# Kernel tuning notes

Measured on AMD Instinct MI355X. Metric: run time of the kernel, lower is better.

The kernel has to match this reference:

```python
import jax, jax.numpy as jnp
import numpy as np

GRID_SIZE = 5
K = 3  # spline order
WIDTH = [512, 1024, 1024, 1024, 256]
BATCH = 4096


def make_grid(in_dim):
    # pykan-style extended uniform grid on [-1, 1]: G + 2K + 1 knots per input dim
    h = 2.0 / GRID_SIZE
    pts = jnp.arange(-K, GRID_SIZE + K + 1, dtype=jnp.float32) * h - 1.0
    return jnp.tile(pts[None, :], (in_dim, 1))


def bspline_basis(x, grid):
    # Cox-de Boor recursion. x: [B, in], grid: [in, G+2K+1] -> basis [B, in, G+K]
    xe = x[..., None]
    b = ((xe >= grid[:, :-1]) & (xe < grid[:, 1:])).astype(x.dtype)  # degree 0: [B, in, G+2K]
    for d in range(1, K + 1):
        left = (xe - grid[:, :-(d + 1)]) / (grid[:, d:-1] - grid[:, :-(d + 1)]) * b[..., :-1]
        right = (grid[:, d + 1:] - xe) / (grid[:, d + 1:] - grid[:, 1:-d]) * b[..., 1:]
        b = left + right
    return b


def kan_layer(x, grid, coef, scale_base, scale_sp):
    # out_j = sum_i scale_base[i,j]*silu(x_i) + scale_sp[i,j]*sum_g coef[i,j,g]*B_g(x_i)
    basis = bspline_basis(x, grid)                                   # [B, in, G+K]
    base = jnp.einsum('bi,io->bo', jax.nn.silu(x), scale_base)
    spline = jnp.einsum('big,iog->bo', basis, coef * scale_sp[:, :, None])
    return base + spline


def setup_inputs() -> dict:
    key = jax.random.key(0)
    n_layers = len(WIDTH) - 1
    keys = jax.random.split(key, 2 + 2 * n_layers)
    inp = {
        'inputs_y': jax.random.normal(keys[0], (BATCH, 256), dtype=jnp.float32) * 0.5,
        'inputs_u': jax.random.normal(keys[1], (BATCH, 256), dtype=jnp.float32) * 0.5,
    }
    for l, (din, dout) in enumerate(zip(WIDTH[:-1], WIDTH[1:])):
        inp[f'coef{l}'] = jax.random.normal(keys[2 + 2 * l], (din, dout, GRID_SIZE + K), dtype=jnp.float32) * (0.1 / np.sqrt(din))
        inp[f'sb{l}'] = jax.random.normal(keys[3 + 2 * l], (din, dout), dtype=jnp.float32) * (1.0 / np.sqrt(din))
        inp[f'ss{l}'] = jnp.ones((din, dout), dtype=jnp.float32)
        inp[f'grid{l}'] = make_grid(din)
    return inp


def reference(inputs_y, inputs_u,
              coef0, sb0, ss0, grid0,
              coef1, sb1, ss1, grid1,
              coef2, sb2, ss2, grid2,
              coef3, sb3, ss3, grid3):
    x = jnp.concatenate([inputs_y.astype(jnp.float32), inputs_u.astype(jnp.float32)], axis=-1)
    layers = [(grid0, coef0, sb0, ss0), (grid1, coef1, sb1, ss1),
              (grid2, coef2, sb2, ss2), (grid3, coef3, sb3, ss3)]
    for g, c, sb, ss in layers:
        x = kan_layer(x, g, c, sb, ss)
    return x
```

## Files before the change

### kernel.cpp

```cpp
#include <hip/hip_runtime.h>
#include <cstdint>
#include <cstddef>

typedef _Float16 f16;
typedef _Float16 f16x4 __attribute__((ext_vector_type(4)));
typedef _Float16 f16x8 __attribute__((ext_vector_type(8)));
typedef float f32x4 __attribute__((ext_vector_type(4)));

__device__ __forceinline__ void gl2lds16(const void* g, void* l) {
  __builtin_amdgcn_global_load_lds(
      (const __attribute__((address_space(1))) void*)(uintptr_t)g,
      (__attribute__((address_space(3))) void*)(uintptr_t)l,
      16, 0, 0);
}

__global__ __launch_bounds__(256) void kan_prep2(
    const float* __restrict__ coef, const float* __restrict__ sb,
    const float* __restrict__ ss, f16* __restrict__ Wt,
    int out, int K9)
{
  __shared__ float s_sb[32][32];
  __shared__ float s_ss[32][32];
  __shared__ f16 s_w[32][288];
  const int t  = threadIdx.x;
  const int o0 = blockIdx.x * 32, i0 = blockIdx.y * 32;

  {
    int il = t >> 3, oc = (t & 7) * 4;
    float4 vb = *(const float4*)(sb + (size_t)(i0 + il) * out + o0 + oc);
    float4 vs = *(const float4*)(ss + (size_t)(i0 + il) * out + o0 + oc);
    s_sb[il][oc + 0] = vb.x; s_sb[il][oc + 1] = vb.y;
    s_sb[il][oc + 2] = vb.z; s_sb[il][oc + 3] = vb.w;
    s_ss[il][oc + 0] = vs.x; s_ss[il][oc + 1] = vs.y;
    s_ss[il][oc + 2] = vs.z; s_ss[il][oc + 3] = vs.w;
  }
  __syncthreads();

#pragma unroll
  for (int j = 0; j < 8; ++j) {
    int f  = j * 256 + t;
    int il = f >> 6, c = f & 63;
    int ol = c >> 1, gh = (c & 1) * 4;
    float4 v = *(const float4*)(coef + ((size_t)(i0 + il) * out + (o0 + ol)) * 8 + gh);
    float ssv = s_ss[il][ol];
    f16* dst = &s_w[ol][il * 9 + 1 + gh];
    dst[0] = (f16)(v.x * ssv); dst[1] = (f16)(v.y * ssv);
    dst[2] = (f16)(v.z * ssv); dst[3] = (f16)(v.w * ssv);
  }
#pragma unroll
  for (int j = 0; j < 4; ++j) {
    int e = j * 256 + t; int il = e >> 5, ol = e & 31;
    s_w[ol][il * 9] = (f16)s_sb[il][ol];
  }
  __syncthreads();

  {
    int o = t >> 3, part = t & 7;
    f16* dst = Wt + (size_t)(o0 + o) * K9 + (size_t)i0 * 9 + part * 36;
    const f16* src = &s_w[o][part * 36];
#pragma unroll
    for (int q = 0; q < 9; ++q)
      *(f16x4*)(dst + q * 4) = *(const f16x4*)(src + q * 4);
  }
}

__global__ __launch_bounds__(256) void kan_feat(
    const float* __restrict__ X, f16* __restrict__ F,
    int shift, int K9, int iBase)
{
  int idx = blockIdx.x * 256 + threadIdx.x;
  int b  = idx >> shift;
  int ii = idx & ((1 << shift) - 1);
  float x = X[idx];

  float sig  = 1.0f / (1.0f + __expf(-x));
  float silu = x * sig;

  float t[12];
#pragma unroll
  for (int j = 0; j < 12; ++j) t[j] = (float)(j - 3) * 0.4f - 1.0f;
  float b0[11];
#pragma unroll
  for (int j = 0; j < 11; ++j)
    b0[j] = (x >= t[j] && x < t[j + 1]) ? 1.0f : 0.0f;
  float b1[10];
#pragma unroll
  for (int j = 0; j < 10; ++j)
    b1[j] = (x - t[j]) * 2.5f * b0[j] + (t[j + 2] - x) * 2.5f * b0[j + 1];
  float b2[9];
#pragma unroll
  for (int j = 0; j < 9; ++j)
    b2[j] = (x - t[j]) * 1.25f * b1[j] + (t[j + 3] - x) * 1.25f * b1[j + 1];
  float b3[8];
#pragma unroll
  for (int j = 0; j < 8; ++j)
    b3[j] = (x - t[j]) * (1.0f / 1.2f) * b2[j] +
            (t[j + 4] - x) * (1.0f / 1.2f) * b2[j + 1];

  f16* o = F + (size_t)b * K9 + (size_t)(iBase + ii) * 9;
  o[0] = (f16)silu;
#pragma unroll
  for (int g = 0; g < 8; ++g) o[1 + g] = (f16)b3[g];
}

template <int SPLITK>
__global__ __launch_bounds__(512, 2) void kan_gemm(
    const f16* __restrict__ A, const f16* __restrict__ Bt,
    float* __restrict__ C, int N, int K)
{
  __shared__ __align__(16) f16 lds[4][16384];
  const int tid   = threadIdx.x;
  const int lane  = tid & 63;
  const int w     = tid >> 6;
  const int waveM = w >> 2, waveN = w & 3;
  const int l16   = lane & 15, quad = lane >> 4;
  const size_t mBase = (size_t)blockIdx.y * 256;
  const size_t nBase = (size_t)blockIdx.x * 256;
  const int kChunk = K / SPLITK;
  const int k0     = blockIdx.z * kChunk;
  const int kSteps = kChunk >> 5;

  const f16* gA[2]; int lA[2];
  const f16* gB[2]; int lB[2];
#pragma unroll
  for (int r = 0; r < 2; ++r) {
    int g = r * 512 + tid, row = g >> 2;
    int cs = (g & 3) ^ ((row >> 1) & 3);
    gA[r] = A + (mBase + row) * (size_t)K + k0 + cs * 8;
    gB[r] = Bt + (nBase + row) * (size_t)K + k0 + cs * 8;
    lA[r] = (r * 512 + (tid & ~63)) * 8;
    lB[r] = 8192 + lA[r];
  }

  f32x4 acc[8][4] = {};

#pragma unroll
  for (int p = 0; p < 3; ++p) {
    f16* b = lds[p];
    int kk = p * 32;
#pragma unroll
    for (int r = 0; r < 2; ++r) {
      gl2lds16(gA[r] + kk, b + lA[r]);
      gl2lds16(gB[r] + kk, b + lB[r]);
    }
  }

  for (int s = 0; s < kSteps; ++s) {
    if (s < kSteps - 2)       asm volatile("s_waitcnt vmcnt(8)" ::: "memory");
    else if (s == kSteps - 2) asm volatile("s_waitcnt vmcnt(4)" ::: "memory");
    else                      asm volatile("s_waitcnt vmcnt(0)" ::: "memory");
    __builtin_amdgcn_s_barrier();

    if (s + 3 < kSteps) {
      int kk = (s + 3) * 32;
      f16* b = lds[(s + 3) & 3];
#pragma unroll
      for (int r = 0; r < 2; ++r) {
        gl2lds16(gA[r] + kk, b + lA[r]);
        gl2lds16(gB[r] + kk, b + lB[r]);
      }
    }

    const f16* buf = lds[s & 3];
    f16x8 af[8], bf[4];
#pragma unroll
    for (int mi = 0; mi < 8; ++mi) {
      int row = waveM * 128 + mi * 16 + l16;
      af[mi] = *(const f16x8*)(buf + row * 32 + (quad ^ ((row >> 1) & 3)) * 8);
    }
#pragma unroll
    for (int ni = 0; ni < 4; ++ni) {
      int col = waveN * 64 + ni * 16 + l16;
      bf[ni] = *(const f16x8*)(buf + 8192 + col * 32 + (quad ^ ((col >> 1) & 3)) * 8);
    }
#pragma unroll
    for (int mi = 0; mi < 8; ++mi)
#pragma unroll
      for (int ni = 0; ni < 4; ++ni)
        acc[mi][ni] = __builtin_amdgcn_mfma_f32_16x16x32_f16(
            af[mi], bf[ni], acc[mi][ni], 0, 0, 0);
  }

#pragma unroll
  for (int mi = 0; mi < 8; ++mi) {
    size_t row = mBase + waveM * 128 + mi * 16 + quad * 4;
#pragma unroll
    for (int ni = 0; ni < 4; ++ni) {
      size_t col = nBase + waveN * 64 + ni * 16 + l16;
#pragma unroll
      for (int r = 0; r < 4; ++r)
        unsafeAtomicAdd(C + (row + r) * N + col, acc[mi][ni][r]);
    }
  }
}

extern "C" void kernel_launch(void* const* d_in, const int* in_sizes, int n_in,
                              void* d_out, int out_size, void* d_ws, size_t ws_size,
                              hipStream_t stream)
{
  const float* y = (const float*)d_in[0];
  const float* u = (const float*)d_in[1];
  const float* coef[4]; const float* sb[4]; const float* ss[4];
  for (int l = 0; l < 4; ++l) {
    coef[l] = (const float*)d_in[2 + 4 * l];
    sb[l]   = (const float*)d_in[3 + 4 * l];
    ss[l]   = (const float*)d_in[4 + 4 * l];
  }
  char* ws = (char*)d_ws;
  f16*   Wt   = (f16*)(ws);
  f16*   F    = (f16*)(ws + 18874368);
  float* actA = (float*)(ws + 18874368 + 75497472);
  float* actB = (float*)(ws + 18874368 + 75497472 + 16777216);
  float* out  = (float*)d_out;
  const size_t actBytes = (size_t)4096 * 1024 * 4;

  kan_prep2<<<dim3(32, 16), 256, 0, stream>>>(coef[0], sb[0], ss[0], Wt, 1024, 4608);
  kan_feat<<<4096 * 256 / 256, 256, 0, stream>>>(y, F, 8, 4608, 0);
  kan_feat<<<4096 * 256 / 256, 256, 0, stream>>>(u, F, 8, 4608, 256);
  hipMemsetAsync(actA, 0, actBytes, stream);
  kan_gemm<4><<<dim3(4, 16, 4), 512, 0, stream>>>(F, Wt, actA, 1024, 4608);

  kan_prep2<<<dim3(32, 32), 256, 0, stream>>>(coef[1], sb[1], ss[1], Wt, 1024, 9216);
  kan_feat<<<4096 * 1024 / 256, 256, 0, stream>>>(actA, F, 10, 9216, 0);
  hipMemsetAsync(actB, 0, actBytes, stream);
  kan_gemm<4><<<dim3(4, 16, 4), 512, 0, stream>>>(F, Wt, actB, 1024, 9216);

  kan_prep2<<<dim3(32, 32), 256, 0, stream>>>(coef[2], sb[2], ss[2], Wt, 1024, 9216);
  kan_feat<<<4096 * 1024 / 256, 256, 0, stream>>>(actB, F, 10, 9216, 0);
  hipMemsetAsync(actA, 0, actBytes, stream);
  kan_gemm<4><<<dim3(4, 16, 4), 512, 0, stream>>>(F, Wt, actA, 1024, 9216);

  kan_prep2<<<dim3(8, 32), 256, 0, stream>>>(coef[3], sb[3], ss[3], Wt, 256, 9216);
  kan_feat<<<4096 * 1024 / 256, 256, 0, stream>>>(actA, F, 10, 9216, 0);
  hipMemsetAsync(d_out, 0, (size_t)out_size * sizeof(float), stream);
  kan_gemm<16><<<dim3(1, 16, 16), 512, 0, stream>>>(F, Wt, out, 256, 9216);
}
```

Before: 670.9 us.

## Restructure split-K GEMM main loop into 64-wide K tiles with quarter-step MFMA scheduling

Replaces the 4-stage, 32-wide-K LDS ring with a double-buffered 64-wide-K tile. Each tile is processed in four quarter MFMA blocks, and barriers plus raised wave priority interleave the global-to-LDS loads, LDS fragment reads and MFMAs. The aim is to overlap memory staging with tensor-core work and cut per-step barrier and wait overhead, using an 8-column XOR swizzle to avoid LDS bank conflicts. The last layer's split-K drops from 16 to 12, which means fewer atomic-add passes but fewer blocks. The many barriers per tile, and requiring an even tile count, add risk.

Result: faster. 635.7 us (-5.2%).

```diff
diff --git a/kernel.cpp b/kernel.cpp
--- a/kernel.cpp
+++ b/kernel.cpp
@@ -103,82 +103,121 @@
   for (int g = 0; g < 8; ++g) o[1 + g] = (f16)b3[g];
 }
 
+#define BARRIER() do { asm volatile("" ::: "memory"); \
+    __builtin_amdgcn_s_barrier(); asm volatile("" ::: "memory"); } while (0)
+#define LGKM0() asm volatile("s_waitcnt lgkmcnt(0)" ::: "memory")
+#define VMC4()  asm volatile("s_waitcnt vmcnt(4)" ::: "memory")
+#define VMC0()  asm volatile("s_waitcnt vmcnt(0)" ::: "memory")
+
+#define STG_A(h, tile) do { size_t _o = (size_t)(h) * hK + (size_t)(tile) * 64; \
+    f16* _d = L + ((((tile) & 1) << 15) + ((h) << 13)); \
+    gl2lds16(gA[0] + _o, _d + stO0); gl2lds16(gA[1] + _o, _d + stO1); } while (0)
+#define STG_B(h, tile) do { size_t _o = (size_t)(h) * hK + (size_t)(tile) * 64; \
+    f16* _d = L + ((((tile) & 1) << 15) + 16384 + ((h) << 13)); \
+    gl2lds16(gB[0] + _o, _d + stO0); gl2lds16(gB[1] + _o, _d + stO1); } while (0)
+
+#define RD_ALO(pa) do { _Pragma("unroll") for (int i = 0; i < 4; ++i) { \
+    a[2*i]   = *(const f16x8*)((pa) + i * 1024 + fo0); \
+    a[2*i+1] = *(const f16x8*)((pa) + i * 1024 + fo1); } } while (0)
+#define RD_AHI(pa) do { _Pragma("unroll") for (int i = 0; i < 4; ++i) { \
+    a[2*i]   = *(const f16x8*)((pa) + 4096 + i * 1024 + fo0); \
+    a[2*i+1] = *(const f16x8*)((pa) + 4096 + i * 1024 + fo1); } } while (0)
+#define RD_BLO(pb) do { _Pragma("unroll") for (int i = 0; i < 2; ++i) { \
+    b[2*i]   = *(const f16x8*)((pb) + i * 1024 + fo0); \
+    b[2*i+1] = *(const f16x8*)((pb) + i * 1024 + fo1); } } while (0)
+#define RD_BHI(pb) do { _Pragma("unroll") for (int i = 0; i < 2; ++i) { \
+    b[4+2*i] = *(const f16x8*)((pb) + (2 + i) * 1024 + fo0); \
+    b[5+2*i] = *(const f16x8*)((pb) + (2 + i) * 1024 + fo1); } } while (0)
+
+#define MFMA_Q(MH, NH) do { \
+  __builtin_amdgcn_s_setprio(1); \
+  _Pragma("unroll") for (int kk = 0; kk < 2; ++kk) \
+  _Pragma("unroll") for (int mi = 0; mi < 4; ++mi) \
+  _Pragma("unroll") for (int ni = 0; ni < 2; ++ni) \
+    acc[(MH)*4+mi][(NH)*2+ni] = __builtin_amdgcn_mfma_f32_16x16x32_f16( \
+        a[2*mi+kk], b[2*((NH)*2+ni)+kk], acc[(MH)*4+mi][(NH)*2+ni], 0, 0, 0); \
+  __builtin_amdgcn_s_setprio(0); } while (0)
+
 template <int SPLITK>
-__global__ __launch_bounds__(512, 2) void kan_gemm(
+__global__ __launch_bounds__(512, 2) void kan_gemm8(
     const f16* __restrict__ A, const f16* __restrict__ Bt,
     float* __restrict__ C, int N, int K)
 {
-  __shared__ __align__(16) f16 lds[4][16384];
-  const int tid   = threadIdx.x;
-  const int lane  = tid & 63;
-  const int w     = tid >> 6;
+  __shared__ __align__(16) f16 lds[65536];
+  f16* L = lds;
+  const int tid  = threadIdx.x;
+  const int lane = tid & 63;
+  const int w    = tid >> 6;
   const int waveM = w >> 2, waveN = w & 3;
-  const int l16   = lane & 15, quad = lane >> 4;
+  const int l16 = lane & 15, quad = lane >> 4;
   const size_t mBase = (size_t)blockIdx.y * 256;
   const size_t nBase = (size_t)blockIdx.x * 256;
   const int kChunk = K / SPLITK;
-  const int k0     = blockIdx.z * kChunk;
-  const int kSteps = kChunk >> 5;
-
-  const f16* gA[2]; int lA[2];
-  const f16* gB[2]; int lB[2];
-#pragma unroll
-  for (int r = 0; r < 2; ++r) {
-    int g = r * 512 + tid, row = g >> 2;
-    int cs = (g & 3) ^ ((row >> 1) & 3);
-    gA[r] = A + (mBase + row) * (size_t)K + k0 + cs * 8;
-    gB[r] = Bt + (nBase + row) * (size_t)K + k0 + cs * 8;
-    lA[r] = (r * 512 + (tid & ~63)) * 8;
-    lB[r] = 8192 + lA[r];
-  }
+  const int k0  = blockIdx.z * kChunk;
+  const int nkt = kChunk >> 6;
+  const size_t hK = 128 * (size_t)K;
+
+  const f16* gA[2]; const f16* gB[2];
+  {
+    int c0 = tid,        r0 = c0 >> 3, p0 = c0 & 7;
+    int c1 = 512 + tid,  r1 = c1 >> 3, p1 = c1 & 7;
+    gA[0] = A  + (mBase + r0) * (size_t)K + k0 + (p0 ^ ((r0 >> 1) & 7)) * 8;
+    gA[1] = A  + (mBase + r1) * (size_t)K + k0 + (p1 ^ ((r1 >> 1) & 7)) * 8;
+    gB[0] = Bt + (nBase + r0) * (size_t)K + k0 + (p0 ^ ((r0 >> 1) & 7)) * 8;
+    gB[1] = Bt + (nBase + r1) * (size_t)K + k0 + (p1 ^ ((r1 >> 1) & 7)) * 8;
+  }
+  const int stO0 = (tid & ~63) * 8;
+  const int stO1 = (512 + (tid & ~63)) * 8;
+
+  const int s3  = l16 >> 1;
+  const int fo0 = l16 * 64 + ((quad ^ s3) & 7) * 8;
+  const int fo1 = l16 * 64 + (((quad + 4) ^ s3) & 7) * 8;
+  const int slotA = waveM * 8192;
+  const int slotB = 16384 + (waveN >> 1) * 8192 + (waveN & 1) * 4096;
 
   f32x4 acc[8][4] = {};
 
-#pragma unroll
-  for (int p = 0; p < 3; ++p) {
-    f16* b = lds[p];
-    int kk = p * 32;
-#pragma unroll
-    for (int r = 0; r < 2; ++r) {
-      gl2lds16(gA[r] + kk, b + lA[r]);
-      gl2lds16(gB[r] + kk, b + lB[r]);
+  STG_A(0, 0); STG_A(1, 0); STG_B(0, 0); STG_B(1, 0);
+  STG_B(0, 1); STG_B(1, 1);
+  VMC4();
+  BARRIER();
+
+#pragma unroll 1
+  for (int it = 0; it < (nkt >> 1); ++it) {
+    const int t = it * 2;
+    const bool nl = (t + 2) < nkt;
+    f16x8 a[8], b[8];
+
+    {
+      const f16* pa = L + ((t & 1) << 15) + slotA;
+      const f16* pb = L + ((t & 1) << 15) + slotB;
+      RD_ALO(pa); RD_BLO(pb);
+      STG_A(0, t + 1);
+      BARRIER(); LGKM0(); MFMA_Q(0, 0); BARRIER();
+      RD_BHI(pb);
+      STG_A(1, t + 1);
+      BARRIER(); LGKM0(); MFMA_Q(0, 1); BARRIER();
+      RD_AHI(pa);
+      if (nl) STG_B(0, t + 2);
+      BARRIER(); LGKM0(); MFMA_Q(1, 1); BARRIER();
+      if (nl) { STG_B(1, t + 2); VMC4(); } else { VMC0(); }
+      BARRIER(); MFMA_Q(1, 0); BARRIER();
     }
-  }
-
-  for (int s = 0; s < kSteps; ++s) {
-    if (s < kSteps - 2)       asm volatile("s_waitcnt vmcnt(8)" ::: "memory");
-    else if (s == kSteps - 2) asm volatile("s_waitcnt vmcnt(4)" ::: "memory");
-    else                      asm volatile("s_waitcnt vmcnt(0)" ::: "memory");
-    __builtin_amdgcn_s_barrier();
-
-    if (s + 3 < kSteps) {
-      int kk = (s + 3) * 32;
-      f16* b = lds[(s + 3) & 3];
-#pragma unroll
-      for (int r = 0; r < 2; ++r) {
-        gl2lds16(gA[r] + kk, b + lA[r]);
-        gl2lds16(gB[r] + kk, b + lB[r]);
-      }
+    {
+      const f16* pa = L + (((t + 1) & 1) << 15) + slotA;
+      const f16* pb = L + (((t + 1) & 1) << 15) + slotB;
+      RD_ALO(pa); RD_BLO(pb);
+      if (nl) STG_A(0, t + 2);
+      BARRIER(); LGKM0(); MFMA_Q(0, 0); BARRIER();
+      RD_BHI(pb);
+      if (nl) STG_A(1, t + 2);
+      BARRIER(); LGKM0(); MFMA_Q(0, 1); BARRIER();
+      RD_AHI(pa);
+      if (nl) STG_B(0, t + 3);
+      BARRIER(); LGKM0(); MFMA_Q(1, 1); BARRIER();
+      if (nl) { STG_B(1, t + 3); VMC4(); } else { VMC0(); }
+      BARRIER(); MFMA_Q(1, 0); BARRIER();
     }
-
-    const f16* buf = lds[s & 3];
-    f16x8 af[8], bf[4];
-#pragma unroll
-    for (int mi = 0; mi < 8; ++mi) {
-      int row = waveM * 128 + mi * 16 + l16;
-      af[mi] = *(const f16x8*)(buf + row * 32 + (quad ^ ((row >> 1) & 3)) * 8);
-    }
-#pragma unroll
-    for (int ni = 0; ni < 4; ++ni) {
-      int col = waveN * 64 + ni * 16 + l16;
-      bf[ni] = *(const f16x8*)(buf + 8192 + col * 32 + (quad ^ ((col >> 1) & 3)) * 8);
-    }
-#pragma unroll
-    for (int mi = 0; mi < 8; ++mi)
-#pragma unroll
-      for (int ni = 0; ni < 4; ++ni)
-        acc[mi][ni] = __builtin_amdgcn_mfma_f32_16x16x32_f16(
-            af[mi], bf[ni], acc[mi][ni], 0, 0, 0);
   }
 
 #pragma unroll
@@ -218,20 +257,20 @@
   kan_feat<<<4096 * 256 / 256, 256, 0, stream>>>(y, F, 8, 4608, 0);
   kan_feat<<<4096 * 256 / 256, 256, 0, stream>>>(u, F, 8, 4608, 256);
   hipMemsetAsync(actA, 0, actBytes, stream);
-  kan_gemm<4><<<dim3(4, 16, 4), 512, 0, stream>>>(F, Wt, actA, 1024, 4608);
+  kan_gemm8<4><<<dim3(4, 16, 4), 512, 0, stream>>>(F, Wt, actA, 1024, 4608);
 
   kan_prep2<<<dim3(32, 32), 256, 0, stream>>>(coef[1], sb[1], ss[1], Wt, 1024, 9216);
   kan_feat<<<4096 * 1024 / 256, 256, 0, stream>>>(actA, F, 10, 9216, 0);
   hipMemsetAsync(actB, 0, actBytes, stream);
-  kan_gemm<4><<<dim3(4, 16, 4), 512, 0, stream>>>(F, Wt, actB, 1024, 9216);
+  kan_gemm8<4><<<dim3(4, 16, 4), 512, 0, stream>>>(F, Wt, actB, 1024, 9216);
 
   kan_prep2<<<dim3(32, 32), 256, 0, stream>>>(coef[2], sb[2], ss[2], Wt, 1024, 9216);
   kan_feat<<<4096 * 1024 / 256, 256, 0, stream>>>(actB, F, 10, 9216, 0);
   hipMemsetAsync(actA, 0, actBytes, stream);
-  kan_gemm<4><<<dim3(4, 16, 4), 512, 0, stream>>>(F, Wt, actA, 1024, 9216);
+  kan_gemm8<4><<<dim3(4, 16, 4), 512, 0, stream>>>(F, Wt, actA, 1024, 9216);
 
   kan_prep2<<<dim3(8, 32), 256, 0, stream>>>(coef[3], sb[3], ss[3], Wt, 256, 9216);
   kan_feat<<<4096 * 1024 / 256, 256, 0, stream>>>(actA, F, 10, 9216, 0);
   hipMemsetAsync(d_out, 0, (size_t)out_size * sizeof(float), stream);
-  kan_gemm<16><<<dim3(1, 16, 16), 512, 0, stream>>>(F, Wt, out, 256, 9216);
-}
+  kan_gemm8<12><<<dim3(1, 16, 12), 512, 0, stream>>>(F, Wt, out, 256, 9216);
+}
```
